# Kernel optimization log

Hardware: AMD Instinct MI355X
Metric: run time of the kernel (lower is better)

## Reference

```python
import jax, jax.numpy as jnp
import numpy as np

B, S, ENC = 64, 2048, 1024          # batch, encoder seq len, encoder feature dim
U, E_DIM, V_SZ = 512, 256, 50000    # dec_units, embedding_dim, vocab_size
IN_DIM = ENC + E_DIM                # LSTM input: [context ; token embedding]


def setup_inputs() -> dict:
    key = jax.random.key(0)
    ks = jax.random.split(key, 16)
    g = lambda k, shp, s=0.02: (jax.random.normal(k, shp, jnp.float32) * s)
    return {
        "x": jax.random.randint(ks[0], (B, 1), 0, V_SZ),
        "c_fwd": g(ks[1], (B, U), 0.1),
        "c_bwd": g(ks[2], (B, U), 0.1),
        "enc_output": jax.random.normal(ks[3], (B, S, ENC), jnp.float32),
        "emb": g(ks[4], (V_SZ, E_DIM)),
        "W1_w": g(ks[5], (ENC, U)), "W1_b": jnp.zeros((U,), jnp.float32),
        "W2_w": g(ks[6], (U, U)),   "W2_b": jnp.zeros((U,), jnp.float32),
        "W3_w": g(ks[7], (U, U)),   "W3_b": jnp.zeros((U,), jnp.float32),
        "V_w": g(ks[8], (U, 1)),    "V_b": jnp.zeros((1,), jnp.float32),
        "Kf": g(ks[9], (IN_DIM, 4 * U)),  "bf": jnp.zeros((4 * U,), jnp.float32),
        "Kb": g(ks[10], (IN_DIM, 4 * U)), "bb": jnp.zeros((4 * U,), jnp.float32),
        "fc_w": g(ks[11], (2 * U, V_SZ)), "fc_b": jnp.zeros((V_SZ,), jnp.float32),
    }


def _lstm_step_zero_state(xin, K, b):
    # Keras LSTM single step from zero (h0, c0): recurrent term vanishes.
    # Gate order in Keras kernel: i, f, c(g), o.
    z = xin @ K + b
    i, f, g, o = jnp.split(z, 4, axis=-1)
    i, o = jax.nn.sigmoid(i), jax.nn.sigmoid(o)  # f gate multiplies c0=0
    c = i * jnp.tanh(g)
    h = o * jnp.tanh(c)
    return h, c


def reference(x, c_fwd, c_bwd, enc_output, emb,
              W1_w, W1_b, W2_w, W2_b, W3_w, W3_b, V_w, V_b,
              Kf, bf, Kb, bb, fc_w, fc_b):
    # Bahdanau additive attention: score [B, S, 1]
    hidden_proj = (c_fwd @ W2_w + W2_b + c_bwd @ W3_w + W3_b)[:, None, :]  # [B,1,U]
    score = jnp.tanh(enc_output @ W1_w + W1_b + hidden_proj) @ V_w + V_b
    attn = jax.nn.softmax(score, axis=1)                 # softmax over S
    ctx = jnp.sum(attn * enc_output, axis=1)             # [B, ENC]

    xe = emb[x[:, 0]]                                    # [B, E_DIM]
    xin = jnp.concatenate([ctx, xe], axis=-1)            # [B, ENC+E_DIM]

    # Bidirectional LSTM over a length-1 sequence from zero initial state:
    # both directions see the same single timestep with separate weights.
    hf, cf = _lstm_step_zero_state(xin, Kf, bf)
    hb, cb = _lstm_step_zero_state(xin, Kb, bb)

    out = jnp.concatenate([hf, hb], axis=-1)             # [B, 2U]
    logits = out @ fc_w + fc_b                           # [B, vocab]
    return logits, hf, cf, hb, cb
```

## Files before the change

kernel.cpp:

```cpp
#include <hip/hip_runtime.h>

using u16 = unsigned short;
typedef float f32x4 __attribute__((ext_vector_type(4)));
typedef __bf16 bf16x8 __attribute__((ext_vector_type(8)));
typedef u16 u16x8 __attribute__((ext_vector_type(8)));
typedef u16 u16x4 __attribute__((ext_vector_type(4)));

static constexpr int OF_HPB   = 262144;
static constexpr int OF_CTXP  = 294912;
static constexpr int OF_STATS = 2392064;
static constexpr int OF_XIN   = 2394112;
static constexpr int OF_ZPART = 2476032;
static constexpr int OF_HHL   = 3000320;
static constexpr size_t SCRATCH_FLOATS = 3065856;
static constexpr size_t SCRATCH_BYTES  = SCRATCH_FLOATS * 4ull;

__device__ __forceinline__ u16 f2bf(float f) {
  unsigned u = __float_as_uint(f);
  u += 0x7FFFu + ((u >> 16) & 1u);
  return (u16)(u >> 16);
}
__device__ __forceinline__ float bf2f(u16 u) {
  return __uint_as_float((unsigned)u << 16);
}
__device__ __forceinline__ float fast_tanh(float x) {
  x = fminf(fmaxf(x, -20.f), 20.f);
  float e = __expf(2.f * x);
  return (e - 1.f) / (e + 1.f);
}
__device__ __forceinline__ float fast_sig(float x) { return 1.f / (1.f + __expf(-x)); }

__device__ __forceinline__ void gll16(const u16* g, u16* l) {
  __builtin_amdgcn_global_load_lds(
      (const __attribute__((address_space(1))) unsigned int*)g,
      (__attribute__((address_space(3))) unsigned int*)l, 16, 0, 0);
}

__global__ void k_prep_w1(const float* __restrict__ W1w, u16* __restrict__ w1p) {
  __shared__ float tile[32][132];
  const int t = threadIdx.x;
  const int ks = blockIdx.x >> 2, u0 = (blockIdx.x & 3) * 128;
  {
    int kk = t >> 3, ui = (t & 7) * 16;
    const float* src = W1w + (size_t)(ks * 32 + kk) * 512 + u0 + ui;
    #pragma unroll
    for (int i = 0; i < 4; ++i)
      *(float4*)&tile[kk][ui + i * 4] = *(const float4*)(src + i * 4);
  }
  __syncthreads();
  {
    int u = t >> 1, kh = (t & 1) * 16;
    u16x8 p0, p1;
    #pragma unroll
    for (int i = 0; i < 8; ++i) {
      p0[i] = f2bf(tile[kh + i][u]);
      p1[i] = f2bf(tile[kh + 8 + i][u]);
    }
    u16* dst = w1p + ((size_t)ks * 512 + u0 + u) * 32 + kh;
    *(u16x8*)(dst)     = p0;
    *(u16x8*)(dst + 8) = p1;
  }
}

__global__ void k_prep_hp(const float* __restrict__ cf, const float* __restrict__ cb,
                          const float* __restrict__ W2w, const float* __restrict__ W2b,
                          const float* __restrict__ W3w, const float* __restrict__ W3b,
                          const float* __restrict__ W1b, float* __restrict__ hpb) {
  __shared__ float cfl[512], cbl[512];
  const int b = blockIdx.x, t = threadIdx.x;
  cfl[t] = cf[(size_t)b * 512 + t];       cfl[t + 256] = cf[(size_t)b * 512 + t + 256];
  cbl[t] = cb[(size_t)b * 512 + t];       cbl[t + 256] = cb[(size_t)b * 512 + t + 256];
  __syncthreads();
  const int u1 = t, u2 = t + 256;
  float a1 = W2b[u1] + W3b[u1] + W1b[u1];
  float a2 = W2b[u2] + W3b[u2] + W1b[u2];
  for (int k = 0; k < 512; ++k) {
    float c1 = cfl[k], c2 = cbl[k];
    const float* r2 = W2w + (size_t)k * 512;
    const float* r3 = W3w + (size_t)k * 512;
    a1 += c1 * r2[u1] + c2 * r3[u1];
    a2 += c1 * r2[u2] + c2 * r3[u2];
  }
  hpb[(size_t)b * 512 + u1] = a1;
  hpb[(size_t)b * 512 + u2] = a2;
}

__global__ void __launch_bounds__(512, 4)
k_attn(const float* __restrict__ enc, const u16* __restrict__ w1p,
       const float* __restrict__ hpb, const float* __restrict__ Vw,
       const float* __restrict__ Vb, float* __restrict__ ctxp,
       float* __restrict__ stats) {
  __shared__ __align__(16) u16 smem[36864];

  const int t = threadIdx.x;
  const int bid = blockIdx.x;
  const int b = bid >> 5, tile = bid & 31;
  const size_t row0 = (size_t)b * 2048 + (size_t)tile * 64;

  const int l = t & 63, w = t >> 6;
  const int ln = l & 15, lg = l >> 4;

  const int s_im = t >> 7, s_ln = (t >> 3) & 15, s_lg = (t >> 1) & 3, s_h = t & 1;
  const float* a_src = enc + (row0 + s_im * 16 + s_ln) * 1024 + s_lg * 8 + s_h * 4;
  const int a_dst = (s_im * 64 + s_lg * 16 + s_ln) * 8 + s_h * 4;
  const u16* bsrc = w1p + (size_t)(w * 64 + ln) * 32 + lg * 8;
  u16* bdst = smem + w * 2048;

  f32x4 acc[4][4];
  #pragma unroll
  for (int im = 0; im < 4; ++im)
    #pragma unroll
    for (int nf = 0; nf < 4; ++nf) acc[im][nf] = f32x4{0.f, 0.f, 0.f, 0.f};

  float4 avB;
  {
    float4 av0 = *(const float4*)(a_src);
    u16x4 aw;
    aw[0]=f2bf(av0.x); aw[1]=f2bf(av0.y); aw[2]=f2bf(av0.z); aw[3]=f2bf(av0.w);
    *(u16x4*)(smem + 32768 + a_dst) = aw;
    gll16(bsrc,        bdst);
    gll16(bsrc +  512, bdst +  512);
    gll16(bsrc + 1024, bdst + 1024);
    gll16(bsrc + 1536, bdst + 1536);
    avB = *(const float4*)(a_src + 32);
  }
  __syncthreads();

  for (int ks = 0; ks < 32; ++ks) {
    const int cur = ks & 1;
    if (ks < 31) {
      u16* An = smem + 32768 + ((cur ^ 1) << 11);
      u16x4 aw;
      aw[0]=f2bf(avB.x); aw[1]=f2bf(avB.y); aw[2]=f2bf(avB.z); aw[3]=f2bf(avB.w);
      *(u16x4*)(An + a_dst) = aw;
      if (ks < 30) avB = *(const float4*)(a_src + (ks + 2) * 32);
      u16* bd = bdst + ((cur ^ 1) << 14);
      const u16* bs = bsrc + (size_t)(ks + 1) * 16384;
      gll16(bs, bd);               gll16(bs +  512, bd +  512);
      gll16(bs + 1024, bd + 1024); gll16(bs + 1536, bd + 1536);
    }
    const u16* Ac = smem + 32768 + (cur << 11);
    const u16* Bc = smem + (cur << 14) + w * 2048;
    bf16x8 afr[4], bfr[4];
    #pragma unroll
    for (int im = 0; im < 4; ++im) afr[im] = *(const bf16x8*)(Ac + im * 512 + l * 8);
    #pragma unroll
    for (int nf = 0; nf < 4; ++nf) bfr[nf] = *(const bf16x8*)(Bc + nf * 512 + l * 8);
    #pragma unroll
    for (int im = 0; im < 4; ++im)
      #pragma unroll
      for (int nf = 0; nf < 4; ++nf)
        acc[im][nf] = __builtin_amdgcn_mfma_f32_16x16x32_bf16(afr[im], bfr[nf], acc[im][nf], 0, 0, 0);
    __syncthreads();
  }

  float* fsm = (float*)smem;
  float* red = fsm;
  float* scv = fsm + 576;
  float* pcv = fsm + 640;

  float vw_l[4], hp_l[4];
  #pragma unroll
  for (int nf = 0; nf < 4; ++nf) {
    int col = w * 64 + nf * 16 + ln;
    vw_l[nf] = Vw[col];
    hp_l[nf] = hpb[(size_t)b * 512 + col];
  }
  #pragma unroll
  for (int im = 0; im < 4; ++im) {
    #pragma unroll
    for (int r = 0; r < 4; ++r) {
      float s = 0.f;
      #pragma unroll
      for (int nf = 0; nf < 4; ++nf)
        s += vw_l[nf] * fast_tanh(acc[im][nf][r] + hp_l[nf]);
      s += __shfl_xor(s, 1);
      s += __shfl_xor(s, 2);
      s += __shfl_xor(s, 4);
      s += __shfl_xor(s, 8);
      if (ln == 0) red[(im * 16 + lg * 4 + r) * 9 + w] = s;
    }
  }
  __syncthreads();
  if (t < 64) {
    float s = Vb[0];
    #pragma unroll
    for (int w2 = 0; w2 < 8; ++w2) s += red[t * 9 + w2];
    float e = __expf(s);
    scv[t] = e;
    float p = e;
    p += __shfl_xor(p, 1);  p += __shfl_xor(p, 2);  p += __shfl_xor(p, 4);
    p += __shfl_xor(p, 8);  p += __shfl_xor(p, 16); p += __shfl_xor(p, 32);
    if (t == 0) stats[bid] = p;
  }
  __syncthreads();

  {
    const int c4 = (t & 255) * 4;
    const int rh = t >> 8;
    const float* ep = enc + (row0 + rh * 32) * 1024 + c4;
    float ax = 0.f, ay = 0.f, az = 0.f, aw2 = 0.f;
    #pragma unroll 4
    for (int r = 0; r < 32; ++r) {
      float4 v = *(const float4*)(ep + (size_t)r * 1024);
      float s = scv[rh * 32 + r];
      ax += s * v.x; ay += s * v.y; az += s * v.z; aw2 += s * v.w;
    }
    if (t >= 256) {
      float4 st = {ax, ay, az, aw2};
      *(float4*)&pcv[c4] = st;
    }
    __syncthreads();
    if (t < 256) {
      float4 p2 = *(const float4*)&pcv[c4];
      float4 o = {ax + p2.x, ay + p2.y, az + p2.z, aw2 + p2.w};
      *(float4*)&ctxp[(size_t)bid * 1024 + c4] = o;
    }
  }
}

__global__ void k_attn_reduce(const float* __restrict__ ctxp, const float* __restrict__ stats,
                              const int* __restrict__ x, const float* __restrict__ emb,
                              float* __restrict__ xin) {
  __shared__ float ps[32];
  __shared__ float invs;
  const int b = blockIdx.x, t = threadIdx.x;
  if (t < 32) ps[t] = stats[b * 32 + t];
  __syncthreads();
  if (t == 0) {
    float s = 0.f;
    #pragma unroll
    for (int i = 0; i < 32; ++i) s += ps[i];
    invs = 1.f / s;
  }
  __syncthreads();
  const float inv = invs;
  #pragma unroll
  for (int i = 0; i < 4; ++i) {
    int c = t + i * 256;
    float a = 0.f;
    for (int chv = 0; chv < 32; ++chv)
      a += ctxp[((size_t)b * 32 + chv) * 1024 + c];
    xin[(size_t)b * 1280 + c] = a * inv;
  }
  xin[(size_t)b * 1280 + 1024 + t] = emb[(size_t)x[b] * 256 + t];
}

__global__ void k_lstm_gemm(const float* __restrict__ xin, const float* __restrict__ Kf,
                            const float* __restrict__ Kb, float* __restrict__ zpart) {
  __shared__ float xl[32][68];
  const int t = threadIdx.x;
  const int bid = blockIdx.x;
  const int dir = bid >> 7;
  const int jt  = (bid >> 1) & 63;
  const int ks  = bid & 1;
  const float* K = dir ? Kb : Kf;
  const int j  = jt * 32 + (t & 31);
  const int tb = t >> 5;
  const int brow = t >> 2, kq = (t & 3) * 8;
  float acc[8] = {0,0,0,0,0,0,0,0};
  for (int k0 = ks * 640; k0 < ks * 640 + 640; k0 += 32) {
    float4 x0 = *(const float4*)&xin[(size_t)brow * 1280 + k0 + kq];
    float4 x1 = *(const float4*)&xin[(size_t)brow * 1280 + k0 + kq + 4];
    __syncthreads();
    xl[kq+0][brow]=x0.x; xl[kq+1][brow]=x0.y; xl[kq+2][brow]=x0.z; xl[kq+3][brow]=x0.w;
    xl[kq+4][brow]=x1.x; xl[kq+5][brow]=x1.y; xl[kq+6][brow]=x1.z; xl[kq+7][brow]=x1.w;
    __syncthreads();
    const float* Kp = K + (size_t)k0 * 2048 + j;
    #pragma unroll 8
    for (int kk = 0; kk < 32; ++kk) {
      float wv = Kp[(size_t)kk * 2048];
      float4 v0 = *(const float4*)&xl[kk][tb * 8];
      float4 v1 = *(const float4*)&xl[kk][tb * 8 + 4];
      acc[0] += v0.x * wv; acc[1] += v0.y * wv; acc[2] += v0.z * wv; acc[3] += v0.w * wv;
      acc[4] += v1.x * wv; acc[5] += v1.y * wv; acc[6] += v1.z * wv; acc[7] += v1.w * wv;
    }
  }
  float* zp = zpart + ((size_t)dir * 2 + ks) * 64 * 2048;
  #pragma unroll
  for (int i = 0; i < 8; ++i)
    zp[(size_t)(tb * 8 + i) * 2048 + j] = acc[i];
}

__global__ void k_gates(const float* __restrict__ zpart, const float* __restrict__ bfv,
                        const float* __restrict__ bbv, float* __restrict__ dout,
                        u16* __restrict__ hhl) {
  const int dir = blockIdx.x >> 6, b = blockIdx.x & 63, u = threadIdx.x;
  const float* bias = dir ? bbv : bfv;
  const float* z0 = zpart + ((size_t)dir * 2 + 0) * 131072 + (size_t)b * 2048;
  const float* z1 = zpart + ((size_t)dir * 2 + 1) * 131072 + (size_t)b * 2048;
  float zi = z0[u]        + z1[u]        + bias[u];
  float zg = z0[1024 + u] + z1[1024 + u] + bias[1024 + u];
  float zo = z0[1536 + u] + z1[1536 + u] + bias[1536 + u];
  float c = fast_sig(zi) * fast_tanh(zg);
  float h = fast_sig(zo) * fast_tanh(c);
  size_t base = 3200000u + (size_t)dir * 65536u;
  dout[base + (size_t)b * 512 + u] = h;
  dout[base + 32768u + (size_t)b * 512 + u] = c;
  u16 hi = f2bf(h);
  u16 lo = f2bf(h - bf2f(hi));
  hhl[(size_t)b * 1024 + dir * 512 + u] = hi;
  hhl[65536u + (size_t)b * 1024 + dir * 512 + u] = lo;
}

__global__ void __launch_bounds__(256)
k_fc_mfma(const float* __restrict__ fcw, const u16* __restrict__ hhl,
          const float* __restrict__ fcb, float* __restrict__ logits) {
  __shared__ float Bs[2][32 * 136];
  const int t = threadIdx.x;
  const int j0 = blockIdx.x * 128;
  const int l = t & 63, w = t >> 6;
  const int ln = l & 15, lg = l >> 4;
  const int srow = t >> 3, scol = (t & 7) * 16;
  const bool interior = (j0 + 128 <= 50000);

  f32x4 acc[4][2];
  #pragma unroll
  for (int im = 0; im < 4; ++im)
    #pragma unroll
    for (int nf = 0; nf < 2; ++nf) acc[im][nf] = f32x4{0.f, 0.f, 0.f, 0.f};

  float4 pre[4];
  {
    const float* src = fcw + (size_t)srow * 50000 + j0 + scol;
    if (interior) {
      #pragma unroll
      for (int q = 0; q < 4; ++q) pre[q] = *(const float4*)(src + q * 4);
    } else {
      #pragma unroll
      for (int q = 0; q < 4; ++q) {
        int jb = j0 + scol + q * 4;
        pre[q].x = (jb + 0 < 50000) ? src[q*4 + 0] : 0.f;
        pre[q].y = (jb + 1 < 50000) ? src[q*4 + 1] : 0.f;
        pre[q].z = (jb + 2 < 50000) ? src[q*4 + 2] : 0.f;
        pre[q].w = (jb + 3 < 50000) ? src[q*4 + 3] : 0.f;
      }
    }
    #pragma unroll
    for (int q = 0; q < 4; ++q)
      *(float4*)&Bs[0][srow * 136 + scol + q * 4] = pre[q];
  }
  __syncthreads();

  for (int ks = 0; ks < 32; ++ks) {
    const int cur = ks & 1;
    if (ks < 31) {
      const float* src = fcw + (size_t)(ks + 1) * 32 * 50000 + (size_t)srow * 50000 + j0 + scol;
      if (interior) {
        #pragma unroll
        for (int q = 0; q < 4; ++q) pre[q] = *(const float4*)(src + q * 4);
      } else {
        #pragma unroll
        for (int q = 0; q < 4; ++q) {
          int jb = j0 + scol + q * 4;
          pre[q].x = (jb + 0 < 50000) ? src[q*4 + 0] : 0.f;
          pre[q].y = (jb + 1 < 50000) ? src[q*4 + 1] : 0.f;
          pre[q].z = (jb + 2 < 50000) ? src[q*4 + 2] : 0.f;
          pre[q].w = (jb + 3 < 50000) ? src[q*4 + 3] : 0.f;
        }
      }
    }
    bf16x8 ahi[4], alo[4];
    #pragma unroll
    for (int im = 0; im < 4; ++im) {
      const u16* ha = hhl + (size_t)(im * 16 + ln) * 1024 + ks * 32 + lg * 8;
      ahi[im] = *(const bf16x8*)(ha);
      alo[im] = *(const bf16x8*)(ha + 65536);
    }
    bf16x8 bfr[2];
    #pragma unroll
    for (int nf = 0; nf < 2; ++nf) {
      u16x8 pv;
      #pragma unroll
      for (int i = 0; i < 8; ++i)
        pv[i] = f2bf(Bs[cur][(lg * 8 + i) * 136 + w * 32 + nf * 16 + ln]);
      bfr[nf] = *(bf16x8*)&pv;
    }
    #pragma unroll
    for (int im = 0; im < 4; ++im)
      #pragma unroll
      for (int nf = 0; nf < 2; ++nf) {
        acc[im][nf] = __builtin_amdgcn_mfma_f32_16x16x32_bf16(alo[im], bfr[nf], acc[im][nf], 0, 0, 0);
        acc[im][nf] = __builtin_amdgcn_mfma_f32_16x16x32_bf16(ahi[im], bfr[nf], acc[im][nf], 0, 0, 0);
      }
    if (ks < 31) {
      #pragma unroll
      for (int q = 0; q < 4; ++q)
        *(float4*)&Bs[cur ^ 1][srow * 136 + scol + q * 4] = pre[q];
    }
    __syncthreads();
  }

  #pragma unroll
  for (int nf = 0; nf < 2; ++nf) {
    int c = j0 + w * 32 + nf * 16 + ln;
    if (c < 50000) {
      float fb = fcb[c];
      #pragma unroll
      for (int im = 0; im < 4; ++im)
        #pragma unroll
        for (int r = 0; r < 4; ++r) {
          int row = im * 16 + lg * 4 + r;
          logits[(size_t)row * 50000 + c] = acc[im][nf][r] + fb;
        }
    }
  }
}

__global__ void __launch_bounds__(256)
k_fc_f32(const float* __restrict__ dout_ro, const float* __restrict__ fcw,
         const float* __restrict__ fcb, float* __restrict__ logits) {
  __shared__ float ol[64][68];
  __shared__ float wl[64][132];
  const int t = threadIdx.x;
  const int j0 = blockIdx.x * 128;
  const int tb = t >> 5, tj = t & 31;
  const float* hf = dout_ro + 3200000u;
  const float* hb = dout_ro + 3200000u + 65536u;
  float acc[8][4];
  #pragma unroll
  for (int bi = 0; bi < 8; ++bi)
    #pragma unroll
    for (int ji = 0; ji < 4; ++ji) acc[bi][ji] = 0.f;

  for (int k0 = 0; k0 < 1024; k0 += 64) {
    __syncthreads();
    {
      int bb = t >> 2, kq = (t & 3) * 16;
      const float* src = (k0 < 512) ? (hf + (size_t)bb * 512 + k0 + kq)
                                    : (hb + (size_t)bb * 512 + (k0 - 512) + kq);
      #pragma unroll
      for (int i = 0; i < 4; ++i) {
        float4 v = *(const float4*)(src + i * 4);
        ol[kq + i*4 + 0][bb] = v.x;
        ol[kq + i*4 + 1][bb] = v.y;
        ol[kq + i*4 + 2][bb] = v.z;
        ol[kq + i*4 + 3][bb] = v.w;
      }
    }
    {
      int kk = t >> 2, jh = (t & 3) * 32;
      const float* wsrc = fcw + (size_t)(k0 + kk) * 50000 + j0 + jh;
      #pragma unroll
      for (int i = 0; i < 8; ++i) {
        int j = j0 + jh + i * 4;
        float4 v;
        if (j + 3 < 50000) {
          v = *(const float4*)(wsrc + i * 4);
        } else {
          v.x = (j + 0 < 50000) ? wsrc[i*4 + 0] : 0.f;
          v.y = (j + 1 < 50000) ? wsrc[i*4 + 1] : 0.f;
          v.z = (j + 2 < 50000) ? wsrc[i*4 + 2] : 0.f;
          v.w = 0.f;
        }
        *(float4*)&wl[kk][jh + i * 4] = v;
      }
    }
    __syncthreads();
    #pragma unroll 4
    for (int kk = 0; kk < 64; ++kk) {
      float4 wv = *(const float4*)&wl[kk][tj * 4];
      float4 q0 = *(const float4*)&ol[kk][tb * 8];
      float4 q1 = *(const float4*)&ol[kk][tb * 8 + 4];
      float obv[8] = {q0.x, q0.y, q0.z, q0.w, q1.x, q1.y, q1.z, q1.w};
      #pragma unroll
      for (int bi = 0; bi < 8; ++bi) {
        acc[bi][0] += obv[bi] * wv.x;
        acc[bi][1] += obv[bi] * wv.y;
        acc[bi][2] += obv[bi] * wv.z;
        acc[bi][3] += obv[bi] * wv.w;
      }
    }
  }

  const int j = j0 + tj * 4;
  if (j + 3 < 50000) {
    float4 fb = *(const float4*)(fcb + j);
    #pragma unroll
    for (int bi = 0; bi < 8; ++bi) {
      float4 r;
      r.x = acc[bi][0] + fb.x; r.y = acc[bi][1] + fb.y;
      r.z = acc[bi][2] + fb.z; r.w = acc[bi][3] + fb.w;
      *(float4*)&logits[(size_t)(tb * 8 + bi) * 50000 + j] = r;
    }
  } else {
    for (int ji = 0; ji < 4; ++ji) {
      if (j + ji < 50000) {
        float fb = fcb[j + ji];
        for (int bi = 0; bi < 8; ++bi)
          logits[(size_t)(tb * 8 + bi) * 50000 + j + ji] = acc[bi][ji] + fb;
      }
    }
  }
}

extern "C" void kernel_launch(void* const* d_in, const int* in_sizes, int n_in,
                              void* d_out, int out_size, void* d_ws, size_t ws_size,
                              hipStream_t stream) {
  const int*   x    = (const int*)  d_in[0];
  const float* cfwd = (const float*)d_in[1];
  const float* cbwd = (const float*)d_in[2];
  const float* enc  = (const float*)d_in[3];
  const float* emb  = (const float*)d_in[4];
  const float* W1w  = (const float*)d_in[5];
  const float* W1b  = (const float*)d_in[6];
  const float* W2w  = (const float*)d_in[7];
  const float* W2b  = (const float*)d_in[8];
  const float* W3w  = (const float*)d_in[9];
  const float* W3b  = (const float*)d_in[10];
  const float* Vw   = (const float*)d_in[11];
  const float* Vb   = (const float*)d_in[12];
  const float* Kf   = (const float*)d_in[13];
  const float* bfv  = (const float*)d_in[14];
  const float* Kb   = (const float*)d_in[15];
  const float* bbv  = (const float*)d_in[16];
  const float* fcw  = (const float*)d_in[17];
  const float* fcb  = (const float*)d_in[18];
  float* out = (float*)d_out;

  const bool haveWs = (ws_size >= SCRATCH_BYTES);
  float* S = haveWs ? (float*)d_ws : out;
  u16*   w1p   = (u16*)S;
  float* hpb   = S + OF_HPB;
  float* ctxp  = S + OF_CTXP;
  float* stats = S + OF_STATS;
  float* xin   = S + OF_XIN;
  float* zpart = S + OF_ZPART;
  u16*   hhl   = (u16*)(S + OF_HHL);

  k_prep_w1<<<128, 256, 0, stream>>>(W1w, w1p);
  k_prep_hp<<<64, 256, 0, stream>>>(cfwd, cbwd, W2w, W2b, W3w, W3b, W1b, hpb);
  k_attn<<<2048, 512, 0, stream>>>(enc, w1p, hpb, Vw, Vb, ctxp, stats);
  k_attn_reduce<<<64, 256, 0, stream>>>(ctxp, stats, x, emb, xin);
  k_lstm_gemm<<<256, 256, 0, stream>>>(xin, Kf, Kb, zpart);
  k_gates<<<128, 512, 0, stream>>>(zpart, bfv, bbv, out, hhl);
  if (haveWs) k_fc_mfma<<<392, 256, 0, stream>>>(fcw, hhl, fcb, out);
  else        k_fc_f32<<<391, 256, 0, stream>>>(out, fcw, fcb, out);
}
```

Measured before the change: 519.7 us.

## Restructure attention GEMM to 32x32x16 MFMA with 16 waves and direct B loads

The attention score GEMM moves from 16x16x32 MFMA tiles with 8 waves to 32x32x16 MFMA with 16 waves per block. The W1 operand is repacked into a per-wave fragment layout so each wave loads its B fragment straight from global memory instead of staging it through LDS with global_load_lds. LDS shrinks to a small double-buffered A tile over 64 K-steps of 16, and the context accumulation is split four ways. This cuts LDS traffic and raises occupancy, but B now comes from global or L2 each step, and the longer loop has more barriers and less reuse per wave.

```diff
diff --git a/kernel.cpp b/kernel.cpp
--- a/kernel.cpp
+++ b/kernel.cpp
@@ -2,6 +2,7 @@
 
 using u16 = unsigned short;
 typedef float f32x4 __attribute__((ext_vector_type(4)));
+typedef float f32x16 __attribute__((ext_vector_type(16)));
 typedef __bf16 bf16x8 __attribute__((ext_vector_type(8)));
 typedef u16 u16x8 __attribute__((ext_vector_type(8)));
 typedef u16 u16x4 __attribute__((ext_vector_type(4)));
@@ -30,35 +31,27 @@
 }
 __device__ __forceinline__ float fast_sig(float x) { return 1.f / (1.f + __expf(-x)); }
 
-__device__ __forceinline__ void gll16(const u16* g, u16* l) {
-  __builtin_amdgcn_global_load_lds(
-      (const __attribute__((address_space(1))) unsigned int*)g,
-      (__attribute__((address_space(3))) unsigned int*)l, 16, 0, 0);
-}
-
 __global__ void k_prep_w1(const float* __restrict__ W1w, u16* __restrict__ w1p) {
-  __shared__ float tile[32][132];
+  __shared__ float tile[16][516];
   const int t = threadIdx.x;
-  const int ks = blockIdx.x >> 2, u0 = (blockIdx.x & 3) * 128;
+  const int ks = blockIdx.x;
   {
-    int kk = t >> 3, ui = (t & 7) * 16;
-    const float* src = W1w + (size_t)(ks * 32 + kk) * 512 + u0 + ui;
-    #pragma unroll
-    for (int i = 0; i < 4; ++i)
-      *(float4*)&tile[kk][ui + i * 4] = *(const float4*)(src + i * 4);
-  }
-  __syncthreads();
-  {
-    int u = t >> 1, kh = (t & 1) * 16;
-    u16x8 p0, p1;
-    #pragma unroll
-    for (int i = 0; i < 8; ++i) {
-      p0[i] = f2bf(tile[kh + i][u]);
-      p1[i] = f2bf(tile[kh + 8 + i][u]);
-    }
-    u16* dst = w1p + ((size_t)ks * 512 + u0 + u) * 32 + kh;
-    *(u16x8*)(dst)     = p0;
-    *(u16x8*)(dst + 8) = p1;
+    int kk = t >> 4, u0 = (t & 15) * 32;
+    const float* src = W1w + (size_t)(ks * 16 + kk) * 512 + u0;
+    #pragma unroll
+    for (int i = 0; i < 8; ++i)
+      *(float4*)&tile[kk][u0 + i * 4] = *(const float4*)(src + i * 4);
+  }
+  __syncthreads();
+  #pragma unroll
+  for (int q = 0; q < 4; ++q) {
+    int c = t + q * 256;
+    int wv = c >> 6, l = c & 63;
+    int u = wv * 32 + (l & 31), koct = l >> 5;
+    u16x8 p;
+    #pragma unroll
+    for (int e = 0; e < 8; ++e) p[e] = f2bf(tile[koct * 8 + e][u]);
+    *(u16x8*)(w1p + (size_t)ks * 8192 + (size_t)c * 8) = p;
   }
 }
 
@@ -85,107 +78,91 @@
   hpb[(size_t)b * 512 + u2] = a2;
 }
 
-__global__ void __launch_bounds__(512, 4)
+__global__ void __launch_bounds__(1024, 8)
 k_attn(const float* __restrict__ enc, const u16* __restrict__ w1p,
        const float* __restrict__ hpb, const float* __restrict__ Vw,
        const float* __restrict__ Vb, float* __restrict__ ctxp,
        float* __restrict__ stats) {
-  __shared__ __align__(16) u16 smem[36864];
+  __shared__ __align__(16) u16 smem[8448];
 
   const int t = threadIdx.x;
   const int bid = blockIdx.x;
   const int b = bid >> 5, tile = bid & 31;
   const size_t row0 = (size_t)b * 2048 + (size_t)tile * 64;
 
-  const int l = t & 63, w = t >> 6;
-  const int ln = l & 15, lg = l >> 4;
-
-  const int s_im = t >> 7, s_ln = (t >> 3) & 15, s_lg = (t >> 1) & 3, s_h = t & 1;
-  const float* a_src = enc + (row0 + s_im * 16 + s_ln) * 1024 + s_lg * 8 + s_h * 4;
-  const int a_dst = (s_im * 64 + s_lg * 16 + s_ln) * 8 + s_h * 4;
-  const u16* bsrc = w1p + (size_t)(w * 64 + ln) * 32 + lg * 8;
-  u16* bdst = smem + w * 2048;
-
-  f32x4 acc[4][4];
-  #pragma unroll
-  for (int im = 0; im < 4; ++im)
-    #pragma unroll
-    for (int nf = 0; nf < 4; ++nf) acc[im][nf] = f32x4{0.f, 0.f, 0.f, 0.f};
-
-  float4 avB;
-  {
-    float4 av0 = *(const float4*)(a_src);
-    u16x4 aw;
-    aw[0]=f2bf(av0.x); aw[1]=f2bf(av0.y); aw[2]=f2bf(av0.z); aw[3]=f2bf(av0.w);
-    *(u16x4*)(smem + 32768 + a_dst) = aw;
-    gll16(bsrc,        bdst);
-    gll16(bsrc +  512, bdst +  512);
-    gll16(bsrc + 1024, bdst + 1024);
-    gll16(bsrc + 1536, bdst + 1536);
-    avB = *(const float4*)(a_src + 32);
-  }
-  __syncthreads();
-
-  for (int ks = 0; ks < 32; ++ks) {
+  const int l = t & 63, wv = t >> 6;
+
+  const u16* bbase = w1p + (size_t)wv * 512 + (size_t)l * 8;
+
+  const int sr = t >> 2, sh = (t >> 1) & 1, sq = t & 1;
+  const float* a_src = enc + (row0 + sr) * 1024 + sh * 8 + sq * 4;
+  const int a_dst = ((sr >> 5) * 64 + (sr & 31) + (sh << 5)) * 8 + sq * 4;
+
+  f32x16 acc0, acc1;
+  #pragma unroll
+  for (int i = 0; i < 16; ++i) { acc0[i] = 0.f; acc1[i] = 0.f; }
+
+  float4 av = {0.f, 0.f, 0.f, 0.f};
+  if (t < 256) {
+    float4 p0 = *(const float4*)(a_src);
+    u16x4 w4;
+    w4[0] = f2bf(p0.x); w4[1] = f2bf(p0.y); w4[2] = f2bf(p0.z); w4[3] = f2bf(p0.w);
+    *(u16x4*)(smem + a_dst) = w4;
+    av = *(const float4*)(a_src + 16);
+  }
+  __syncthreads();
+
+  #pragma unroll 2
+  for (int ks = 0; ks < 64; ++ks) {
     const int cur = ks & 1;
-    if (ks < 31) {
-      u16* An = smem + 32768 + ((cur ^ 1) << 11);
-      u16x4 aw;
-      aw[0]=f2bf(avB.x); aw[1]=f2bf(avB.y); aw[2]=f2bf(avB.z); aw[3]=f2bf(avB.w);
-      *(u16x4*)(An + a_dst) = aw;
-      if (ks < 30) avB = *(const float4*)(a_src + (ks + 2) * 32);
-      u16* bd = bdst + ((cur ^ 1) << 14);
-      const u16* bs = bsrc + (size_t)(ks + 1) * 16384;
-      gll16(bs, bd);               gll16(bs +  512, bd +  512);
-      gll16(bs + 1024, bd + 1024); gll16(bs + 1536, bd + 1536);
-    }
-    const u16* Ac = smem + 32768 + (cur << 11);
-    const u16* Bc = smem + (cur << 14) + w * 2048;
-    bf16x8 afr[4], bfr[4];
-    #pragma unroll
-    for (int im = 0; im < 4; ++im) afr[im] = *(const bf16x8*)(Ac + im * 512 + l * 8);
-    #pragma unroll
-    for (int nf = 0; nf < 4; ++nf) bfr[nf] = *(const bf16x8*)(Bc + nf * 512 + l * 8);
-    #pragma unroll
-    for (int im = 0; im < 4; ++im)
-      #pragma unroll
-      for (int nf = 0; nf < 4; ++nf)
-        acc[im][nf] = __builtin_amdgcn_mfma_f32_16x16x32_bf16(afr[im], bfr[nf], acc[im][nf], 0, 0, 0);
+    float4 nx = av;
+    if (t < 256 && ks < 62) nx = *(const float4*)(a_src + (ks + 2) * 16);
+    if (t < 256 && ks < 63) {
+      u16x4 w4;
+      w4[0] = f2bf(av.x); w4[1] = f2bf(av.y); w4[2] = f2bf(av.z); w4[3] = f2bf(av.w);
+      *(u16x4*)(smem + ((cur ^ 1) << 10) + a_dst) = w4;
+    }
+    bf16x8 bfr = *(const bf16x8*)(bbase + (size_t)ks * 8192);
+    const u16* Ac = smem + (cur << 10);
+    bf16x8 a0 = *(const bf16x8*)(Ac + l * 8);
+    bf16x8 a1 = *(const bf16x8*)(Ac + 512 + l * 8);
+    acc0 = __builtin_amdgcn_mfma_f32_32x32x16_bf16(a0, bfr, acc0, 0, 0, 0);
+    acc1 = __builtin_amdgcn_mfma_f32_32x32x16_bf16(a1, bfr, acc1, 0, 0, 0);
+    av = nx;
     __syncthreads();
   }
 
   float* fsm = (float*)smem;
   float* red = fsm;
-  float* scv = fsm + 576;
-  float* pcv = fsm + 640;
-
-  float vw_l[4], hp_l[4];
-  #pragma unroll
-  for (int nf = 0; nf < 4; ++nf) {
-    int col = w * 64 + nf * 16 + ln;
-    vw_l[nf] = Vw[col];
-    hp_l[nf] = hpb[(size_t)b * 512 + col];
-  }
-  #pragma unroll
-  for (int im = 0; im < 4; ++im) {
-    #pragma unroll
-    for (int r = 0; r < 4; ++r) {
-      float s = 0.f;
-      #pragma unroll
-      for (int nf = 0; nf < 4; ++nf)
-        s += vw_l[nf] * fast_tanh(acc[im][nf][r] + hp_l[nf]);
+  float* scv = fsm + 1088;
+  float* pcv = fsm + 1152;
+
+  const int ucol = (wv << 5) + (l & 31);
+  const float vwv = Vw[ucol];
+  const float hpv = hpb[(size_t)b * 512 + ucol];
+  const int hi4 = (l >> 5) * 4;
+  const bool writer = ((l & 31) == 0);
+  #pragma unroll
+  for (int im = 0; im < 2; ++im) {
+    #pragma unroll
+    for (int r = 0; r < 16; ++r) {
+      float s = vwv * fast_tanh((im ? acc1[r] : acc0[r]) + hpv);
       s += __shfl_xor(s, 1);
       s += __shfl_xor(s, 2);
       s += __shfl_xor(s, 4);
       s += __shfl_xor(s, 8);
-      if (ln == 0) red[(im * 16 + lg * 4 + r) * 9 + w] = s;
+      s += __shfl_xor(s, 16);
+      if (writer) {
+        int sl = im * 32 + (r & 3) + 8 * (r >> 2) + hi4;
+        red[sl * 17 + wv] = s;
+      }
     }
   }
   __syncthreads();
   if (t < 64) {
     float s = Vb[0];
     #pragma unroll
-    for (int w2 = 0; w2 < 8; ++w2) s += red[t * 9 + w2];
+    for (int wq = 0; wq < 16; ++wq) s += red[t * 17 + wq];
     float e = __expf(s);
     scv[t] = e;
     float p = e;
@@ -197,23 +174,26 @@
 
   {
     const int c4 = (t & 255) * 4;
-    const int rh = t >> 8;
-    const float* ep = enc + (row0 + rh * 32) * 1024 + c4;
+    const int rq = t >> 8;
+    const float* ep = enc + (row0 + rq * 16) * 1024 + c4;
     float ax = 0.f, ay = 0.f, az = 0.f, aw2 = 0.f;
     #pragma unroll 4
-    for (int r = 0; r < 32; ++r) {
+    for (int r = 0; r < 16; ++r) {
       float4 v = *(const float4*)(ep + (size_t)r * 1024);
-      float s = scv[rh * 32 + r];
-      ax += s * v.x; ay += s * v.y; az += s * v.z; aw2 += s * v.w;
-    }
-    if (t >= 256) {
+      float sc = scv[rq * 16 + r];
+      ax += sc * v.x; ay += sc * v.y; az += sc * v.z; aw2 += sc * v.w;
+    }
+    if (rq) {
       float4 st = {ax, ay, az, aw2};
-      *(float4*)&pcv[c4] = st;
-    }
-    __syncthreads();
-    if (t < 256) {
-      float4 p2 = *(const float4*)&pcv[c4];
-      float4 o = {ax + p2.x, ay + p2.y, az + p2.z, aw2 + p2.w};
+      *(float4*)&pcv[(rq - 1) * 1024 + c4] = st;
+    }
+    __syncthreads();
+    if (rq == 0) {
+      float4 p1 = *(const float4*)&pcv[c4];
+      float4 p2 = *(const float4*)&pcv[1024 + c4];
+      float4 p3 = *(const float4*)&pcv[2048 + c4];
+      float4 o = {ax + p1.x + p2.x + p3.x, ay + p1.y + p2.y + p3.y,
+                  az + p1.z + p2.z + p3.z, aw2 + p1.w + p2.w + p3.w};
       *(float4*)&ctxp[(size_t)bid * 1024 + c4] = o;
     }
   }
@@ -528,9 +508,9 @@
   float* zpart = S + OF_ZPART;
   u16*   hhl   = (u16*)(S + OF_HHL);
 
-  k_prep_w1<<<128, 256, 0, stream>>>(W1w, w1p);
+  k_prep_w1<<<64, 256, 0, stream>>>(W1w, w1p);
   k_prep_hp<<<64, 256, 0, stream>>>(cfwd, cbwd, W2w, W2b, W3w, W3b, W1b, hpb);
-  k_attn<<<2048, 512, 0, stream>>>(enc, w1p, hpb, Vw, Vb, ctxp, stats);
+  k_attn<<<2048, 1024, 0, stream>>>(enc, w1p, hpb, Vw, Vb, ctxp, stats);
   k_attn_reduce<<<64, 256, 0, stream>>>(ctxp, stats, x, emb, xin);
   k_lstm_gemm<<<256, 256, 0, stream>>>(xin, Kf, Kb, zpart);
   k_gates<<<128, 512, 0, stream>>>(zpart, bfv, bbv, out, hhl);
```

New measurement: 549.7 us. +5.8%, slower.
